# Kernel tuning notes

Hardware: AMD Instinct MI355X
Metric: run time of the kernel (lower is better)

## Reference

```python
import jax, jax.numpy as jnp
import numpy as np

N_NODES = 100000
N_EDGES = 1600000
N_GRAPHS = 512
NEG_SLOPE = 0.2  # PyG GATConv default


def setup_inputs() -> dict:
    key = jax.random.key(0)
    ks = jax.random.split(key, 12)
    x = jax.random.normal(ks[0], (N_NODES, 75), dtype=jnp.float32)
    edge_index = jax.random.randint(ks[1], (2, N_EDGES), 0, N_NODES, dtype=jnp.int64 if jax.config.jax_enable_x64 else jnp.int32)
    batch = jnp.sort(jax.random.randint(ks[2], (N_NODES,), 0, N_GRAPHS, dtype=jnp.int32))
    s = lambda k, shp, fan: jax.random.normal(k, shp, dtype=jnp.float32) * (1.0 / np.sqrt(fan))
    return {
        "x": x, "edge_index": edge_index, "batch": batch,
        "W1": s(ks[3], (75, 64), 75),           # conv1: heads=8, out=8
        "att_src1": s(ks[4], (8, 8), 8),
        "att_dst1": s(ks[5], (8, 8), 8),
        "bias1": jnp.zeros((64,), jnp.float32),
        "W2": s(ks[6], (64, 128), 64),          # conv2: heads=1, out=128
        "att_src2": s(ks[7], (1, 128), 128),
        "att_dst2": s(ks[8], (1, 128), 128),
        "bias2": jnp.zeros((128,), jnp.float32),
        "Wg": s(ks[9], (128, 1), 128),
        "bg": jnp.zeros((1,), jnp.float32),
    }


def _gat_conv(x, src, dst, W, att_src, att_dst, bias, heads, out_ch):
    # x: [N, F_in]; edges src->dst (self-loops already included)
    n = x.shape[0]
    h = (x @ W).reshape(n, heads, out_ch)            # [N, H, C]
    a_src = (h * att_src).sum(-1)                    # [N, H]
    a_dst = (h * att_dst).sum(-1)                    # [N, H]
    e = a_src[src] + a_dst[dst]                      # [E, H]
    e = jax.nn.leaky_relu(e, NEG_SLOPE)
    # segment softmax over incoming edges of each dst node
    emax = jax.ops.segment_max(e, dst, num_segments=n)      # [N, H]
    ee = jnp.exp(e - emax[dst])
    denom = jax.ops.segment_sum(ee, dst, num_segments=n)    # [N, H]
    alpha = ee / denom[dst]                                  # [E, H]
    msg = h[src] * alpha[:, :, None]                          # [E, H, C]
    out = jax.ops.segment_sum(msg, dst, num_segments=n)      # [N, H, C]
    return out.reshape(n, heads * out_ch) + bias


def reference(x, edge_index, batch, W1, att_src1, att_dst1, bias1,
              W2, att_src2, att_dst2, bias2, Wg, bg):
    n = x.shape[0]
    # PyG GATConv adds self-loops by default
    loops = jnp.arange(n, dtype=edge_index.dtype)
    src = jnp.concatenate([edge_index[0], loops])
    dst = jnp.concatenate([edge_index[1], loops])
    # eval mode: dropout is identity
    x2 = jax.nn.elu(_gat_conv(x, src, dst, W1, att_src1, att_dst1, bias1, heads=8, out_ch=8))
    x4 = _gat_conv(x2, src, dst, W2, att_src2, att_dst2, bias2, heads=1, out_ch=128)
    y = jax.ops.segment_sum(x4, batch, num_segments=N_GRAPHS)  # global_add_pool
    return y @ Wg + bg  # [N_GRAPHS, 1]
```

## Files before the change

### kernel.cpp

```cpp
#include <hip/hip_runtime.h>
#include <hip/hip_bf16.h>
#include <math.h>

#define N_NODES 100000
#define N_EDGES 1600000
#define ET (N_EDGES + N_NODES)
#define N_GRAPHS 512
#define NEG_SLOPE 0.2f
#define G2_BLOCKS 1280

#define BSH 7
#define NDB 128
#define NBUCK ((N_NODES + NDB - 1) / NDB)
#define BCAP 2560
#define ABLK 512
#define CHUNK ((ET + ABLK - 1) / ABLK)
#define F1_OFF (ABLK + 3)
#define PRE_GRID (F1_OFF + 1536)
#define SRC_MASK 131071u

#define BINA_SMEM (CHUNK * 4 + NBUCK * 4 * 4 + 4 + 1024)

__device__ __forceinline__ void atomAddF(float* p, float v) { unsafeAtomicAdd(p, v); }
__device__ __forceinline__ float lrelu(float v) { return v >= 0.f ? v : NEG_SLOPE * v; }

__device__ __forceinline__ unsigned short f2bf(float f) {
    unsigned int u = __float_as_uint(f);
    u += 0x7FFFu + ((u >> 16) & 1u);
    return (unsigned short)(u >> 16);
}
__device__ __forceinline__ float bf2f(unsigned short s) { return __uint_as_float(((unsigned int)s) << 16); }
__device__ __forceinline__ float bflo(unsigned int p) { return __uint_as_float(p << 16); }
__device__ __forceinline__ float bfhi(unsigned int p) { return __uint_as_float(p & 0xFFFF0000u); }

__global__ __launch_bounds__(256) void k_pre(
    const int* __restrict__ ei, unsigned* __restrict__ gbuf, int* __restrict__ bcur,
    const float* __restrict__ x, const float* __restrict__ W1,
    const float* __restrict__ as1, const float* __restrict__ ad1,
    const float* __restrict__ W2, const float* __restrict__ as2,
    const float* __restrict__ ad2, const float* __restrict__ Wg,
    const float* __restrict__ b2, const float* __restrict__ bg,
    unsigned short* __restrict__ h1p, unsigned short* __restrict__ a1sh,
    float* __restrict__ a1d, float* __restrict__ wv, float* __restrict__ out)
{
    __shared__ __align__(16) char smem[BINA_SMEM];
    const int t = threadIdx.x;
    const int blk = blockIdx.x;

    if (blk >= ABLK && blk < F1_OFF) {
        const int bb = blk - ABLK;
        if (bb == 0) {
            if (t < 192) {
                int c = t & 63, which = t >> 6;
                const float* v = (which == 0) ? Wg : ((which == 1) ? as2 : ad2);
                float s = 0.f;
                #pragma unroll
                for (int k = 0; k < 128; ++k) s += W2[c * 128 + k] * v[k];
                wv[which * 64 + c] = s;
            } else if (t == 192) {
                float s = 0.f;
                #pragma unroll
                for (int k = 0; k < 128; ++k) s += b2[k] * Wg[k];
                wv[192] = s;
            }
        } else {
            int i = (bb - 1) * 256 + t;
            if (i < N_GRAPHS) out[i] = bg[0];
        }
        return;
    }

    if (blk >= F1_OFF) {
        float (*xs)[76] = (float (*)[76])smem;
        const int g = t >> 6;
        const int c = t & 63;
        const int vb = blk - F1_OFF;
        const int fstride = PRE_GRID - F1_OFF;
        for (int nb = vb; nb < N_NODES / 4; nb += fstride) {
            const int n = nb * 4 + g;
            const float* xr = x + (long)n * 75;
            xs[g][c] = xr[c];
            if (c < 11) xs[g][64 + c] = xr[64 + c];
            __syncthreads();
            float h = 0.f;
            #pragma unroll
            for (int k = 0; k < 75; ++k) h += xs[g][k] * W1[k * 64 + c];
            h1p[(long)n * 64 + c] = f2bf(h);
            const int head = c >> 3, lane = c & 7;
            float vs = h * as1[c];
            float vd = h * ad1[c];
            #pragma unroll
            for (int off = 1; off < 8; off <<= 1) {
                vs += __shfl_xor(vs, off, 64);
                vd += __shfl_xor(vd, off, 64);
            }
            if (lane == 0) { a1sh[n * 8 + head] = f2bf(vs); a1d[n * 8 + head] = vd; }
            __syncthreads();
        }
        return;
    }

    unsigned* pairs = (unsigned*)smem;
    int* hist  = (int*)(smem + CHUNK * 4);
    int* excl  = hist + NBUCK;
    int* gbase = excl + NBUCK + 1;
    int* cnt2  = gbase + NBUCK;
    int* red   = cnt2 + NBUCK;
    const long e0 = (long)blk * CHUNK;
    const int  n  = (int)((e0 + CHUNK <= ET) ? CHUNK : (ET - e0));
    for (int i = t; i < NBUCK; i += 256) { hist[i] = 0; cnt2[i] = 0; }
    __syncthreads();
    for (int i = t; i < n; i += 256) {
        long e = e0 + i;
        int dst = (e < N_EDGES) ? ei[N_EDGES + e] : (int)(e - N_EDGES);
        atomicAdd(&hist[dst >> BSH], 1);
    }
    __syncthreads();
    {
        int lk[4]; int s = 0;
        #pragma unroll
        for (int k = 0; k < 4; ++k) {
            int idx = t * 4 + k;
            int v = (idx < NBUCK) ? hist[idx] : 0;
            lk[k] = s; s += v;
        }
        red[t] = s;
        __syncthreads();
        for (int off = 1; off < 256; off <<= 1) {
            int a = (t >= off) ? red[t - off] : 0;
            __syncthreads();
            red[t] += a;
            __syncthreads();
        }
        int p = red[t] - s;
        #pragma unroll
        for (int k = 0; k < 4; ++k) {
            int idx = t * 4 + k;
            if (idx < NBUCK) excl[idx] = p + lk[k];
        }
    }
    if (t == 0) excl[NBUCK] = n;
    __syncthreads();
    for (int i = t; i < n; i += 256) {
        long e = e0 + i;
        int src, dst;
        if (e < N_EDGES) { src = ei[e]; dst = ei[N_EDGES + e]; }
        else             { src = dst = (int)(e - N_EDGES); }
        int b = dst >> BSH;
        int pos = excl[b] + atomicAdd(&cnt2[b], 1);
        pairs[pos] = ((unsigned)(dst & (NDB - 1)) << 17) | (unsigned)src;
    }
    __syncthreads();
    for (int b = t; b < NBUCK; b += 256)
        gbase[b] = hist[b] ? atomicAdd(&bcur[b], hist[b]) : 0;
    __syncthreads();
    for (int b = t; b < NBUCK; b += 256) {
        const int s = excl[b], e2 = excl[b + 1];
        if (s == e2) continue;
        unsigned* gp = gbuf + (long)b * BCAP + gbase[b];
        for (int i = s; i < e2; ++i) gp[i - s] = pairs[i];
    }
}

#define SLOT_INIT(k) \
    bool v##k = (k < dgl); \
    int s##k = v##k ? lds_src[beg + k] : 0; \
    unsigned short ab##k = a1sh[(long)s##k * 8 + l]; \
    uint4 pv##k = *(const uint4*)(h1p + (long)s##k * 64 + l * 8);

#define SLOT_STEP(k) { \
    float ee = v##k ? __expf(lrelu(bf2f(ab##k) + adh)) : 0.f; \
    den += ee; \
    acc[0] += ee * bflo(pv##k.x); acc[1] += ee * bfhi(pv##k.x); \
    acc[2] += ee * bflo(pv##k.y); acc[3] += ee * bfhi(pv##k.y); \
    acc[4] += ee * bflo(pv##k.z); acc[5] += ee * bfhi(pv##k.z); \
    acc[6] += ee * bflo(pv##k.w); acc[7] += ee * bfhi(pv##k.w); \
    v##k = (j + 5 + k) < dgl; \
    int sn = v##k ? lds_src[beg + j + 5 + k] : 0; \
    ab##k = a1sh[(long)sn * 8 + l]; \
    pv##k = *(const uint4*)(h1p + (long)sn * 64 + l * 8); }

__global__ __launch_bounds__(512) void k_gat1(
    const unsigned* __restrict__ gbuf, const int* __restrict__ bcur,
    int* __restrict__ rowptr, int* __restrict__ ecol,
    const unsigned short* __restrict__ a1sh, const float* __restrict__ a1d,
    const unsigned short* __restrict__ h1p, const float* __restrict__ bias1,
    const float* __restrict__ wv,
    float2* __restrict__ sg2, float* __restrict__ a2dv)
{
    __shared__ int lds_src[BCAP];
    __shared__ int hist[NDB], excl[NDB + 1], cnt2[NDB];
    __shared__ int red[512];
    const int t = threadIdx.x;
    const int b = blockIdx.x;
    const int d0 = b << BSH;
    const int nloc = (N_NODES - d0 < NDB) ? (N_NODES - d0) : NDB;
    int cntr = bcur[b];
    const int cnt = cntr < BCAP ? cntr : BCAP;

    int partial = 0;
    for (int i = t; i < b; i += 512) partial += bcur[i];
    red[t] = partial;
    __syncthreads();
    for (int off = 256; off > 0; off >>= 1) {
        if (t < off) red[t] += red[t + off];
        __syncthreads();
    }
    const int base = red[0];
    __syncthreads();

    if (t < NDB) { hist[t] = 0; cnt2[t] = 0; }
    __syncthreads();
    const unsigned* eb = gbuf + (long)b * BCAP;
    for (int i = t; i < cnt; i += 512) atomicAdd(&hist[eb[i] >> 17], 1);
    __syncthreads();
    {
        int v = (t < NDB) ? hist[t] : 0;
        if (t < NDB) red[t] = v;
        __syncthreads();
        for (int off = 1; off < NDB; off <<= 1) {
            int a = (t < NDB && t >= off) ? red[t - off] : 0;
            __syncthreads();
            if (t < NDB) red[t] += a;
            __syncthreads();
        }
        if (t < nloc) excl[t] = red[t] - v;
        if (t == 0) excl[nloc] = cnt;
    }
    __syncthreads();
    if (t < nloc) rowptr[d0 + t] = base + excl[t];
    if (b == NBUCK - 1 && t == 0) rowptr[N_NODES] = base + cnt;
    for (int i = t; i < cnt; i += 512) {
        unsigned pr = eb[i];
        int dl = (int)(pr >> 17);
        int slot = excl[dl] + atomicAdd(&cnt2[dl], 1);
        lds_src[slot] = (int)(pr & SRC_MASK);
    }
    __syncthreads();
    for (int i = t; i < cnt; i += 512) ecol[base + i] = lds_src[i];

    const int l = t & 7;
    const int gid = t >> 3;
    for (int dl = gid; dl < nloc; dl += 64) {
        const int dst = d0 + dl;
        const int beg = excl[dl];
        const int dgl = excl[dl + 1] - beg;
        const float adh = a1d[(long)dst * 8 + l];

        float acc[8] = {0.f,0.f,0.f,0.f,0.f,0.f,0.f,0.f};
        float den = 0.f;

        SLOT_INIT(0) SLOT_INIT(1) SLOT_INIT(2) SLOT_INIT(3) SLOT_INIT(4)

        for (int j = 0; j < dgl; j += 5) {
            SLOT_STEP(0) SLOT_STEP(1) SLOT_STEP(2) SLOT_STEP(3) SLOT_STEP(4)
        }

        const float inv = 1.f / den;
        float pg = 0.f, ps = 0.f, pd = 0.f;
        #pragma unroll
        for (int k = 0; k < 8; ++k) {
            float vv = acc[k] * inv + bias1[l * 8 + k];
            vv = vv > 0.f ? vv : (__expf(vv) - 1.f);
            pg += vv * wv[l * 8 + k];
            ps += vv * wv[64 + l * 8 + k];
            pd += vv * wv[128 + l * 8 + k];
        }
        #pragma unroll
        for (int off = 1; off < 8; off <<= 1) {
            pg += __shfl_xor(pg, off, 64);
            ps += __shfl_xor(ps, off, 64);
            pd += __shfl_xor(pd, off, 64);
        }
        if (l == 0) { sg2[dst] = make_float2(ps, pg); a2dv[dst] = pd; }
    }
}

__global__ __launch_bounds__(256) void k_gat2(
    const int* __restrict__ rowptr, const int* __restrict__ ecol,
    const float2* __restrict__ sg2, const float* __restrict__ a2dv,
    const float* __restrict__ wv, const int* __restrict__ batch,
    float* __restrict__ out)
{
    const int sl = threadIdx.x & 7;
    const int sgid = ((blockIdx.x * 256 + threadIdx.x) >> 3);
    const int NS = G2_BLOCKS * 32;
    const int per = (N_NODES + NS - 1) / NS;
    const int n0 = sgid * per;
    const int n1 = min(n0 + per, N_NODES);
    const float bc = wv[192];

    float accg = 0.f;
    int curg = -1;
    for (int n = n0; n < n1; ++n) {
        const int beg = rowptr[n], end = rowptr[n + 1];
        const float adv = a2dv[n];
        float num = 0.f, den = 0.f;
        for (int j = beg + sl; j < end; j += 8) {
            int s = ecol[j];
            float2 v = sg2[s];
            float ee = __expf(lrelu(v.x + adv));
            den += ee;
            num += ee * v.y;
        }
        #pragma unroll
        for (int off = 1; off < 8; off <<= 1) {
            den += __shfl_xor(den, off, 64);
            num += __shfl_xor(num, off, 64);
        }
        if (sl == 0) {
            int gr = batch[n];
            if (gr != curg) {
                if (curg >= 0) atomAddF(out + curg, accg);
                curg = gr; accg = 0.f;
            }
            accg += num / den + bc;
        }
    }
    if (sl == 0 && curg >= 0) atomAddF(out + curg, accg);
}

extern "C" void kernel_launch(void* const* d_in, const int* in_sizes, int n_in,
                              void* d_out, int out_size, void* d_ws, size_t ws_size,
                              hipStream_t stream) {
    (void)in_sizes; (void)n_in; (void)out_size; (void)ws_size;
    const float* x     = (const float*)d_in[0];
    const int*   ei    = (const int*)d_in[1];
    const int*   batch = (const int*)d_in[2];
    const float* W1    = (const float*)d_in[3];
    const float* as1   = (const float*)d_in[4];
    const float* ad1   = (const float*)d_in[5];
    const float* b1    = (const float*)d_in[6];
    const float* W2    = (const float*)d_in[7];
    const float* as2   = (const float*)d_in[8];
    const float* ad2   = (const float*)d_in[9];
    const float* b2    = (const float*)d_in[10];
    const float* Wg    = (const float*)d_in[11];
    const float* bg    = (const float*)d_in[12];
    float* out = (float*)d_out;

    const long N = N_NODES;
    char* p = (char*)d_ws;
    int* rowptr = (int*)p;              p += (N + 4)        * sizeof(int);
    int* bcur   = (int*)p;              p += 1024           * sizeof(int);
    int* ecol   = (int*)p;              p += (long)ET       * sizeof(int);
    unsigned* gbuf = (unsigned*)p;      p += (long)NBUCK * BCAP * sizeof(unsigned);
    unsigned short* h1p  = (unsigned short*)p; p += N * 64  * sizeof(unsigned short);
    unsigned short* a1sh = (unsigned short*)p; p += N * 8   * sizeof(unsigned short);
    float* a1d  = (float*)p;            p += N * 8          * sizeof(float);
    float2* sg2 = (float2*)p;           p += N              * sizeof(float2);
    float* a2dv = (float*)p;            p += N              * sizeof(float);
    float* wv   = (float*)p;            p += 256            * sizeof(float);

    hipMemsetAsync(bcur, 0, NBUCK * sizeof(int), stream);
    k_pre <<<PRE_GRID, 256, 0, stream>>>(ei, gbuf, bcur, x, W1, as1, ad1,
                                         W2, as2, ad2, Wg, b2, bg,
                                         h1p, a1sh, a1d, wv, out);
    k_gat1<<<NBUCK, 512, 0, stream>>>(gbuf, bcur, rowptr, ecol,
                                      a1sh, a1d, h1p, b1, wv, sg2, a2dv);
    k_gat2<<<G2_BLOCKS, 256, 0, stream>>>(rowptr, ecol, sg2, a2dv, wv, batch, out);
}
```

Baseline: 265.7 us.

## Tile layer-1 projection over 16 nodes and widen gat2 edge subgroups to 16

The layer-1 linear projection now stages a 16-node tile of x in shared memory with coalesced loads. Each thread computes 4 nodes per output column, so every W1 load is reused four times, and the second barrier per group of 4 nodes goes away. Separately, k_gat2 switches from 8-lane to 16-lane subgroups per destination node and runs more blocks, which puts more parallelism into each node's edge loop at the cost of more idle lanes on low-degree nodes. The float4 shared reads rely on 16-byte alignment of the 76-float rows.

```diff
diff --git a/kernel.cpp b/kernel.cpp
--- a/kernel.cpp
+++ b/kernel.cpp
@@ -7,7 +7,7 @@
 #define ET (N_EDGES + N_NODES)
 #define N_GRAPHS 512
 #define NEG_SLOPE 0.2f
-#define G2_BLOCKS 1280
+#define G2_BLOCKS 2048
 
 #define BSH 7
 #define NDB 128
@@ -17,6 +17,7 @@
 #define CHUNK ((ET + ABLK - 1) / ABLK)
 #define F1_OFF (ABLK + 3)
 #define PRE_GRID (F1_OFF + 1536)
+#define NT16 (N_NODES / 16)
 #define SRC_MASK 131071u
 
 #define BINA_SMEM (CHUNK * 4 + NBUCK * 4 * 4 + 4 + 1024)
@@ -72,30 +73,56 @@
 
     if (blk >= F1_OFF) {
         float (*xs)[76] = (float (*)[76])smem;
-        const int g = t >> 6;
         const int c = t & 63;
+        const int w = t >> 6;
+        const int qb = w * 4;
         const int vb = blk - F1_OFF;
         const int fstride = PRE_GRID - F1_OFF;
-        for (int nb = vb; nb < N_NODES / 4; nb += fstride) {
-            const int n = nb * 4 + g;
-            const float* xr = x + (long)n * 75;
-            xs[g][c] = xr[c];
-            if (c < 11) xs[g][64 + c] = xr[64 + c];
-            __syncthreads();
-            float h = 0.f;
+        for (int tile = vb; tile < NT16; tile += fstride) {
+            const int n0 = tile * 16;
+            __syncthreads();
+            for (int i = t; i < 16 * 75; i += 256) {
+                int nn = i / 75;
+                int kk = i - nn * 75;
+                xs[nn][kk] = x[(long)n0 * 75 + i];
+            }
+            __syncthreads();
+            float h[4] = {0.f, 0.f, 0.f, 0.f};
             #pragma unroll
-            for (int k = 0; k < 75; ++k) h += xs[g][k] * W1[k * 64 + c];
-            h1p[(long)n * 64 + c] = f2bf(h);
+            for (int k4 = 0; k4 < 18; ++k4) {
+                const float w0 = W1[(k4 * 4 + 0) * 64 + c];
+                const float w1 = W1[(k4 * 4 + 1) * 64 + c];
+                const float w2 = W1[(k4 * 4 + 2) * 64 + c];
+                const float w3 = W1[(k4 * 4 + 3) * 64 + c];
+                #pragma unroll
+                for (int q = 0; q < 4; ++q) {
+                    float4 xv = *(const float4*)(&xs[qb + q][k4 * 4]);
+                    h[q] = fmaf(xv.x, w0, h[q]);
+                    h[q] = fmaf(xv.y, w1, h[q]);
+                    h[q] = fmaf(xv.z, w2, h[q]);
+                    h[q] = fmaf(xv.w, w3, h[q]);
+                }
+            }
+            #pragma unroll
+            for (int k = 72; k < 75; ++k) {
+                const float wk = W1[k * 64 + c];
+                #pragma unroll
+                for (int q = 0; q < 4; ++q) h[q] = fmaf(xs[qb + q][k], wk, h[q]);
+            }
             const int head = c >> 3, lane = c & 7;
-            float vs = h * as1[c];
-            float vd = h * ad1[c];
             #pragma unroll
-            for (int off = 1; off < 8; off <<= 1) {
-                vs += __shfl_xor(vs, off, 64);
-                vd += __shfl_xor(vd, off, 64);
-            }
-            if (lane == 0) { a1sh[n * 8 + head] = f2bf(vs); a1d[n * 8 + head] = vd; }
-            __syncthreads();
+            for (int q = 0; q < 4; ++q) {
+                const int n = n0 + qb + q;
+                h1p[(long)n * 64 + c] = f2bf(h[q]);
+                float vs = h[q] * as1[c];
+                float vd = h[q] * ad1[c];
+                #pragma unroll
+                for (int off = 1; off < 8; off <<= 1) {
+                    vs += __shfl_xor(vs, off, 64);
+                    vd += __shfl_xor(vd, off, 64);
+                }
+                if (lane == 0) { a1sh[n * 8 + head] = f2bf(vs); a1d[n * 8 + head] = vd; }
+            }
         }
         return;
     }
@@ -282,9 +309,9 @@
     const float* __restrict__ wv, const int* __restrict__ batch,
     float* __restrict__ out)
 {
-    const int sl = threadIdx.x & 7;
-    const int sgid = ((blockIdx.x * 256 + threadIdx.x) >> 3);
-    const int NS = G2_BLOCKS * 32;
+    const int sl = threadIdx.x & 15;
+    const int sgid = ((blockIdx.x * 256 + threadIdx.x) >> 4);
+    const int NS = G2_BLOCKS * 16;
     const int per = (N_NODES + NS - 1) / NS;
     const int n0 = sgid * per;
     const int n1 = min(n0 + per, N_NODES);
@@ -296,7 +323,7 @@
         const int beg = rowptr[n], end = rowptr[n + 1];
         const float adv = a2dv[n];
         float num = 0.f, den = 0.f;
-        for (int j = beg + sl; j < end; j += 8) {
+        for (int j = beg + sl; j < end; j += 16) {
             int s = ecol[j];
             float2 v = sg2[s];
             float ee = __expf(lrelu(v.x + adv));
@@ -304,7 +331,7 @@
             num += ee * v.y;
         }
         #pragma unroll
-        for (int off = 1; off < 8; off <<= 1) {
+        for (int off = 1; off < 16; off <<= 1) {
             den += __shfl_xor(den, off, 64);
             num += __shfl_xor(num, off, 64);
         }
```

After: 329.4 us. 1.24x slower.

## Fuse GAT layers into cooperative kernel reusing LDS adjacency across grid sync

Applied to the files above, without the earlier changes.

Merges the layer-1 aggregation and layer-2 attention/pooling kernels into one cooperative launch with a grid-wide sync. The per-bucket source lists stay in LDS, so layer 2 no longer writes and rereads rowptr/ecol through global memory, and one launch goes away. NBUCK (782) blocks of 512 threads must all be co-resident for the cooperative launch; if it fails, the code falls back to the old two kernels. The fallback gat2 also moves to 16 lanes per node.

```diff
diff --git a/kernel.cpp b/kernel.cpp
--- a/kernel.cpp
+++ b/kernel.cpp
@@ -1,6 +1,9 @@
 #include <hip/hip_runtime.h>
 #include <hip/hip_bf16.h>
+#include <hip/hip_cooperative_groups.h>
 #include <math.h>
+
+namespace cg = cooperative_groups;
 
 #define N_NODES 100000
 #define N_EDGES 1600000
@@ -180,6 +183,127 @@
     ab##k = a1sh[(long)sn * 8 + l]; \
     pv##k = *(const uint4*)(h1p + (long)sn * 64 + l * 8); }
 
+__global__ __launch_bounds__(512, 8) void k_gat12(
+    const unsigned* __restrict__ gbuf, const int* __restrict__ bcur,
+    const unsigned short* __restrict__ a1sh, const float* __restrict__ a1d,
+    const unsigned short* __restrict__ h1p, const float* __restrict__ bias1,
+    const float* __restrict__ wv,
+    float2* __restrict__ sg2, float* __restrict__ a2dv,
+    const int* __restrict__ batch, float* __restrict__ out)
+{
+    __shared__ int lds_src[BCAP];
+    __shared__ int hist[NDB], excl[NDB + 1], cnt2[NDB];
+    __shared__ int red[512];
+    const int t = threadIdx.x;
+    const int b = blockIdx.x;
+    const int d0 = b << BSH;
+    const int nloc = (N_NODES - d0 < NDB) ? (N_NODES - d0) : NDB;
+    int cntr = bcur[b];
+    const int cnt = cntr < BCAP ? cntr : BCAP;
+
+    if (t < NDB) { hist[t] = 0; cnt2[t] = 0; }
+    __syncthreads();
+    const unsigned* eb = gbuf + (long)b * BCAP;
+    for (int i = t; i < cnt; i += 512) atomicAdd(&hist[eb[i] >> 17], 1);
+    __syncthreads();
+    {
+        int v = (t < NDB) ? hist[t] : 0;
+        if (t < NDB) red[t] = v;
+        __syncthreads();
+        for (int off = 1; off < NDB; off <<= 1) {
+            int a = (t < NDB && t >= off) ? red[t - off] : 0;
+            __syncthreads();
+            if (t < NDB) red[t] += a;
+            __syncthreads();
+        }
+        if (t < nloc) excl[t] = red[t] - v;
+        if (t == 0) excl[nloc] = cnt;
+    }
+    __syncthreads();
+    for (int i = t; i < cnt; i += 512) {
+        unsigned pr = eb[i];
+        int dl = (int)(pr >> 17);
+        int slot = excl[dl] + atomicAdd(&cnt2[dl], 1);
+        lds_src[slot] = (int)(pr & SRC_MASK);
+    }
+    __syncthreads();
+
+    const int l = t & 7;
+    const int gid = t >> 3;
+    for (int dl = gid; dl < nloc; dl += 64) {
+        const int dst = d0 + dl;
+        const int beg = excl[dl];
+        const int dgl = excl[dl + 1] - beg;
+        const float adh = a1d[(long)dst * 8 + l];
+
+        float acc[8] = {0.f,0.f,0.f,0.f,0.f,0.f,0.f,0.f};
+        float den = 0.f;
+
+        SLOT_INIT(0) SLOT_INIT(1) SLOT_INIT(2) SLOT_INIT(3) SLOT_INIT(4)
+
+        for (int j = 0; j < dgl; j += 5) {
+            SLOT_STEP(0) SLOT_STEP(1) SLOT_STEP(2) SLOT_STEP(3) SLOT_STEP(4)
+        }
+
+        const float inv = 1.f / den;
+        float pg = 0.f, ps = 0.f, pd = 0.f;
+        #pragma unroll
+        for (int k = 0; k < 8; ++k) {
+            float vv = acc[k] * inv + bias1[l * 8 + k];
+            vv = vv > 0.f ? vv : (__expf(vv) - 1.f);
+            pg += vv * wv[l * 8 + k];
+            ps += vv * wv[64 + l * 8 + k];
+            pd += vv * wv[128 + l * 8 + k];
+        }
+        #pragma unroll
+        for (int off = 1; off < 8; off <<= 1) {
+            pg += __shfl_xor(pg, off, 64);
+            ps += __shfl_xor(ps, off, 64);
+            pd += __shfl_xor(pd, off, 64);
+        }
+        if (l == 0) { sg2[dst] = make_float2(ps, pg); a2dv[dst] = pd; }
+    }
+
+    __threadfence();
+    cg::this_grid().sync();
+    __threadfence();
+
+    const int sl = t & 15;
+    const int sg = t >> 4;
+    const float bc = wv[192];
+    float accg = 0.f;
+    int curg = -1;
+    for (int q = 0; q < 4; ++q) {
+        const int dl = sg * 4 + q;
+        if (dl >= nloc) break;
+        const int n = d0 + dl;
+        const int beg = excl[dl], end = excl[dl + 1];
+        const float adv = a2dv[n];
+        float num = 0.f, den = 0.f;
+        for (int j = beg + sl; j < end; j += 16) {
+            int s = lds_src[j];
+            float2 v = sg2[s];
+            float ee = __expf(lrelu(v.x + adv));
+            den += ee;
+            num += ee * v.y;
+        }
+        #pragma unroll
+        for (int off = 1; off < 16; off <<= 1) {
+            den += __shfl_xor(den, off, 64);
+            num += __shfl_xor(num, off, 64);
+        }
+        if (sl == 0) {
+            int gr = batch[n];
+            if (gr != curg) {
+                if (curg >= 0) atomAddF(out + curg, accg);
+                curg = gr; accg = 0.f;
+            }
+            accg += num / den + bc;
+        }
+    }
+    if (sl == 0 && curg >= 0) atomAddF(out + curg, accg);
+}
+
 __global__ __launch_bounds__(512) void k_gat1(
     const unsigned* __restrict__ gbuf, const int* __restrict__ bcur,
     int* __restrict__ rowptr, int* __restrict__ ecol,
@@ -282,9 +406,9 @@
     const float* __restrict__ wv, const int* __restrict__ batch,
     float* __restrict__ out)
 {
-    const int sl = threadIdx.x & 7;
-    const int sgid = ((blockIdx.x * 256 + threadIdx.x) >> 3);
-    const int NS = G2_BLOCKS * 32;
+    const int sl = threadIdx.x & 15;
+    const int sgid = ((blockIdx.x * 256 + threadIdx.x) >> 4);
+    const int NS = G2_BLOCKS * 16;
     const int per = (N_NODES + NS - 1) / NS;
     const int n0 = sgid * per;
     const int n1 = min(n0 + per, N_NODES);
@@ -296,7 +420,7 @@
         const int beg = rowptr[n], end = rowptr[n + 1];
         const float adv = a2dv[n];
         float num = 0.f, den = 0.f;
-        for (int j = beg + sl; j < end; j += 8) {
+        for (int j = beg + sl; j < end; j += 16) {
             int s = ecol[j];
             float2 v = sg2[s];
             float ee = __expf(lrelu(v.x + adv));
@@ -304,7 +428,7 @@
             num += ee * v.y;
         }
         #pragma unroll
-        for (int off = 1; off < 8; off <<= 1) {
+        for (int off = 1; off < 16; off <<= 1) {
             den += __shfl_xor(den, off, 64);
             num += __shfl_xor(num, off, 64);
         }
@@ -356,7 +480,23 @@
     k_pre <<<PRE_GRID, 256, 0, stream>>>(ei, gbuf, bcur, x, W1, as1, ad1,
                                          W2, as2, ad2, Wg, b2, bg,
                                          h1p, a1sh, a1d, wv, out);
-    k_gat1<<<NBUCK, 512, 0, stream>>>(gbuf, bcur, rowptr, ecol,
-                                      a1sh, a1d, h1p, b1, wv, sg2, a2dv);
-    k_gat2<<<G2_BLOCKS, 256, 0, stream>>>(rowptr, ecol, sg2, a2dv, wv, batch, out);
+    {
+        const unsigned* gbuf_c = gbuf; const int* bcur_c = bcur;
+        const unsigned short* a1sh_c = a1sh; const float* a1d_c = a1d;
+        const unsigned short* h1p_c = h1p; const float* b1_c = b1;
+        const float* wv_c = wv; float2* sg2_p = sg2; float* a2dv_p = a2dv;
+        const int* batch_c = batch; float* out_p = out;
+        void* args[] = { (void*)&gbuf_c, (void*)&bcur_c, (void*)&a1sh_c,
+                         (void*)&a1d_c, (void*)&h1p_c, (void*)&b1_c,
+                         (void*)&wv_c, (void*)&sg2_p, (void*)&a2dv_p,
+                         (void*)&batch_c, (void*)&out_p };
+        hipError_t err = hipLaunchCooperativeKernel(
+            (const void*)k_gat12, dim3(NBUCK), dim3(512), args, 0, stream);
+        if (err != hipSuccess) {
+            k_gat1<<<NBUCK, 512, 0, stream>>>(gbuf, bcur, rowptr, ecol,
+                                              a1sh, a1d, h1p, b1, wv, sg2, a2dv);
+            k_gat2<<<G2_BLOCKS, 256, 0, stream>>>(rowptr, ecol, sg2, a2dv, wv,
+                                                  batch, out);
+        }
+    }
 }
```

New measurement: 821.3 us. 209% more time.

## Split CSR build from layer-1 gather into separate kernel with one node per 8 lanes

Applied to the files above, without the earlier changes.

The fused bucket-sort plus layer-1 aggregation kernel is split into k_build, which writes the CSR, and k_gath, which handles one destination node per 8-lane group across many small blocks. The gather now reads edge sources from global ecol instead of LDS, and its software pipeline depth drops from 5 to 3. k_gat2 switches from 8 to 16 lanes per node group. The aim is more parallelism and better load balance for the gather, which was bounded by 782 large blocks with LDS pressure. The cost is an extra kernel launch and a global round trip of ecol.

```diff
diff --git a/kernel.cpp b/kernel.cpp
--- a/kernel.cpp
+++ b/kernel.cpp
@@ -162,31 +162,9 @@
     }
 }
 
-#define SLOT_INIT(k) \
-    bool v##k = (k < dgl); \
-    int s##k = v##k ? lds_src[beg + k] : 0; \
-    unsigned short ab##k = a1sh[(long)s##k * 8 + l]; \
-    uint4 pv##k = *(const uint4*)(h1p + (long)s##k * 64 + l * 8);
-
-#define SLOT_STEP(k) { \
-    float ee = v##k ? __expf(lrelu(bf2f(ab##k) + adh)) : 0.f; \
-    den += ee; \
-    acc[0] += ee * bflo(pv##k.x); acc[1] += ee * bfhi(pv##k.x); \
-    acc[2] += ee * bflo(pv##k.y); acc[3] += ee * bfhi(pv##k.y); \
-    acc[4] += ee * bflo(pv##k.z); acc[5] += ee * bfhi(pv##k.z); \
-    acc[6] += ee * bflo(pv##k.w); acc[7] += ee * bfhi(pv##k.w); \
-    v##k = (j + 5 + k) < dgl; \
-    int sn = v##k ? lds_src[beg + j + 5 + k] : 0; \
-    ab##k = a1sh[(long)sn * 8 + l]; \
-    pv##k = *(const uint4*)(h1p + (long)sn * 64 + l * 8); }
-
-__global__ __launch_bounds__(512) void k_gat1(
+__global__ __launch_bounds__(512) void k_build(
     const unsigned* __restrict__ gbuf, const int* __restrict__ bcur,
-    int* __restrict__ rowptr, int* __restrict__ ecol,
-    const unsigned short* __restrict__ a1sh, const float* __restrict__ a1d,
-    const unsigned short* __restrict__ h1p, const float* __restrict__ bias1,
-    const float* __restrict__ wv,
-    float2* __restrict__ sg2, float* __restrict__ a2dv)
+    int* __restrict__ rowptr, int* __restrict__ ecol)
 {
     __shared__ int lds_src[BCAP];
     __shared__ int hist[NDB], excl[NDB + 1], cnt2[NDB];
@@ -238,42 +216,67 @@
     }
     __syncthreads();
     for (int i = t; i < cnt; i += 512) ecol[base + i] = lds_src[i];
-
+}
+
+#define GSLOT_INIT(k) \
+    bool v##k = (k < dgl); \
+    int s##k = v##k ? erow[k] : 0; \
+    unsigned short ab##k = a1sh[(long)s##k * 8 + l]; \
+    uint4 pv##k = *(const uint4*)(h1p + (long)s##k * 64 + l * 8);
+
+#define GSLOT_STEP(k) { \
+    float ee = v##k ? __expf(lrelu(bf2f(ab##k) + adh)) : 0.f; \
+    den += ee; \
+    acc[0] += ee * bflo(pv##k.x); acc[1] += ee * bfhi(pv##k.x); \
+    acc[2] += ee * bflo(pv##k.y); acc[3] += ee * bfhi(pv##k.y); \
+    acc[4] += ee * bflo(pv##k.z); acc[5] += ee * bfhi(pv##k.z); \
+    acc[6] += ee * bflo(pv##k.w); acc[7] += ee * bfhi(pv##k.w); \
+    v##k = (j + 3 + k) < dgl; \
+    int sn = v##k ? erow[j + 3 + k] : 0; \
+    ab##k = a1sh[(long)sn * 8 + l]; \
+    pv##k = *(const uint4*)(h1p + (long)sn * 64 + l * 8); }
+
+__global__ __launch_bounds__(256) void k_gath(
+    const int* __restrict__ rowptr, const int* __restrict__ ecol,
+    const unsigned short* __restrict__ a1sh, const float* __restrict__ a1d,
+    const unsigned short* __restrict__ h1p, const float* __restrict__ bias1,
+    const float* __restrict__ wv,
+    float2* __restrict__ sg2, float* __restrict__ a2dv)
+{
+    const int t = threadIdx.x;
     const int l = t & 7;
-    const int gid = t >> 3;
-    for (int dl = gid; dl < nloc; dl += 64) {
-        const int dst = d0 + dl;
-        const int beg = excl[dl];
-        const int dgl = excl[dl + 1] - beg;
-        const float adh = a1d[(long)dst * 8 + l];
-
-        float acc[8] = {0.f,0.f,0.f,0.f,0.f,0.f,0.f,0.f};
-        float den = 0.f;
-
-        SLOT_INIT(0) SLOT_INIT(1) SLOT_INIT(2) SLOT_INIT(3) SLOT_INIT(4)
-
-        for (int j = 0; j < dgl; j += 5) {
-            SLOT_STEP(0) SLOT_STEP(1) SLOT_STEP(2) SLOT_STEP(3) SLOT_STEP(4)
-        }
-
-        const float inv = 1.f / den;
-        float pg = 0.f, ps = 0.f, pd = 0.f;
-        #pragma unroll
-        for (int k = 0; k < 8; ++k) {
-            float vv = acc[k] * inv + bias1[l * 8 + k];
-            vv = vv > 0.f ? vv : (__expf(vv) - 1.f);
-            pg += vv * wv[l * 8 + k];
-            ps += vv * wv[64 + l * 8 + k];
-            pd += vv * wv[128 + l * 8 + k];
-        }
-        #pragma unroll
-        for (int off = 1; off < 8; off <<= 1) {
-            pg += __shfl_xor(pg, off, 64);
-            ps += __shfl_xor(ps, off, 64);
-            pd += __shfl_xor(pd, off, 64);
-        }
-        if (l == 0) { sg2[dst] = make_float2(ps, pg); a2dv[dst] = pd; }
-    }
+    const int dst = (blockIdx.x * 256 + t) >> 3;
+
+    const int beg = rowptr[dst];
+    const int dgl = rowptr[dst + 1] - beg;
+    const int* __restrict__ erow = ecol + beg;
+    const float adh = a1d[(long)dst * 8 + l];
+
+    float acc[8] = {0.f,0.f,0.f,0.f,0.f,0.f,0.f,0.f};
+    float den = 0.f;
+
+    GSLOT_INIT(0) GSLOT_INIT(1) GSLOT_INIT(2)
+    for (int j = 0; j < dgl; j += 3) {
+        GSLOT_STEP(0) GSLOT_STEP(1) GSLOT_STEP(2)
+    }
+
+    const float inv = 1.f / den;
+    float pg = 0.f, ps = 0.f, pd = 0.f;
+    #pragma unroll
+    for (int k = 0; k < 8; ++k) {
+        float vv = acc[k] * inv + bias1[l * 8 + k];
+        vv = vv > 0.f ? vv : (__expf(vv) - 1.f);
+        pg += vv * wv[l * 8 + k];
+        ps += vv * wv[64 + l * 8 + k];
+        pd += vv * wv[128 + l * 8 + k];
+    }
+    #pragma unroll
+    for (int off = 1; off < 8; off <<= 1) {
+        pg += __shfl_xor(pg, off, 64);
+        ps += __shfl_xor(ps, off, 64);
+        pd += __shfl_xor(pd, off, 64);
+    }
+    if (l == 0) { sg2[dst] = make_float2(ps, pg); a2dv[dst] = pd; }
 }
 
 __global__ __launch_bounds__(256) void k_gat2(
@@ -282,9 +285,9 @@
     const float* __restrict__ wv, const int* __restrict__ batch,
     float* __restrict__ out)
 {
-    const int sl = threadIdx.x & 7;
-    const int sgid = ((blockIdx.x * 256 + threadIdx.x) >> 3);
-    const int NS = G2_BLOCKS * 32;
+    const int sl = threadIdx.x & 15;
+    const int sgid = ((blockIdx.x * 256 + threadIdx.x) >> 4);
+    const int NS = G2_BLOCKS * 16;
     const int per = (N_NODES + NS - 1) / NS;
     const int n0 = sgid * per;
     const int n1 = min(n0 + per, N_NODES);
@@ -296,7 +299,7 @@
         const int beg = rowptr[n], end = rowptr[n + 1];
         const float adv = a2dv[n];
         float num = 0.f, den = 0.f;
-        for (int j = beg + sl; j < end; j += 8) {
+        for (int j = beg + sl; j < end; j += 16) {
             int s = ecol[j];
             float2 v = sg2[s];
             float ee = __expf(lrelu(v.x + adv));
@@ -304,7 +307,7 @@
             num += ee * v.y;
         }
         #pragma unroll
-        for (int off = 1; off < 8; off <<= 1) {
+        for (int off = 1; off < 16; off <<= 1) {
             den += __shfl_xor(den, off, 64);
             num += __shfl_xor(num, off, 64);
         }
@@ -356,7 +359,8 @@
     k_pre <<<PRE_GRID, 256, 0, stream>>>(ei, gbuf, bcur, x, W1, as1, ad1,
                                          W2, as2, ad2, Wg, b2, bg,
                                          h1p, a1sh, a1d, wv, out);
-    k_gat1<<<NBUCK, 512, 0, stream>>>(gbuf, bcur, rowptr, ecol,
-                                      a1sh, a1d, h1p, b1, wv, sg2, a2dv);
+    k_build<<<NBUCK, 512, 0, stream>>>(gbuf, bcur, rowptr, ecol);
+    k_gath<<<N_NODES / 32, 256, 0, stream>>>(rowptr, ecol, a1sh, a1d, h1p, b1,
+                                             wv, sg2, a2dv);
     k_gat2<<<G2_BLOCKS, 256, 0, stream>>>(rowptr, ecol, sg2, a2dv, wv, batch, out);
 }
```

New measurement: 264.5 us. About the same (-0.4%).
